# Kernel tuning notes

Hardware: AMD Instinct MI355X
Metric: run time of the kernel (lower is better)

## Reference

```python
import jax, jax.numpy as jnp
import numpy as np

R_CUT = 5.0
L_MAX = 3
N_MAX = (8, 7, 6, 5)  # n_max per angular order l (Laplacian-eigenstate-like, shrinking with l)
EPS = 1e-12


def _radial_basis(r):
    """r: [E] -> [E, N_MAX[0]] sine radial basis with smooth cosine cutoff.
    R_n(r) = f_cut(r) * sin((n+1) pi r / r_cut) / r, n = 0..n_max-1."""
    n = jnp.arange(1, N_MAX[0] + 1, dtype=r.dtype)  # (n+1)
    fcut = jnp.where(r < R_CUT, 0.5 * (jnp.cos(jnp.pi * r / R_CUT) + 1.0), 0.0)
    rb = jnp.sin(n[None, :] * (jnp.pi / R_CUT) * r[:, None]) / (r[:, None] + EPS)
    return rb * fcut[:, None]


def _spherical_harmonics(v, r):
    """v: [E,3], r: [E] -> tuple of real SH arrays ([E,1],[E,3],[E,5],[E,7]), m = -l..l."""
    ir = 1.0 / (r + EPS)
    x, y, z = v[:, 0] * ir, v[:, 1] * ir, v[:, 2] * ir
    pi = np.pi
    x2, y2, z2 = x * x, y * y, z * z
    # l = 0
    y0 = jnp.full_like(r, 0.5 * np.sqrt(1.0 / pi))[:, None]
    # l = 1
    c1 = np.sqrt(3.0 / (4.0 * pi))
    y1 = jnp.stack([c1 * y, c1 * z, c1 * x], axis=-1)
    # l = 2
    y2b = jnp.stack([
        0.5 * np.sqrt(15.0 / pi) * x * y,
        0.5 * np.sqrt(15.0 / pi) * y * z,
        0.25 * np.sqrt(5.0 / pi) * (2.0 * z2 - x2 - y2),
        0.5 * np.sqrt(15.0 / pi) * x * z,
        0.25 * np.sqrt(15.0 / pi) * (x2 - y2),
    ], axis=-1)
    # l = 3
    y3b = jnp.stack([
        0.25 * np.sqrt(35.0 / (2.0 * pi)) * y * (3.0 * x2 - y2),
        0.5 * np.sqrt(105.0 / pi) * x * y * z,
        0.25 * np.sqrt(21.0 / (2.0 * pi)) * y * (4.0 * z2 - x2 - y2),
        0.25 * np.sqrt(7.0 / pi) * z * (2.0 * z2 - 3.0 * x2 - 3.0 * y2),
        0.25 * np.sqrt(21.0 / (2.0 * pi)) * x * (4.0 * z2 - x2 - y2),
        0.25 * np.sqrt(105.0 / pi) * z * (x2 - y2),
        0.25 * np.sqrt(35.0 / (2.0 * pi)) * x * (x2 - 3.0 * y2),
    ], axis=-1)
    return (y0, y1, y2b, y3b)


def setup_inputs() -> dict:
    key = jax.random.key(0)
    E = 1_000_000
    vectors = 1.5 * jax.random.normal(key, (E, 3), dtype=jnp.float32)
    return {"vectors": vectors}


def reference(vectors):
    # vectors: [E, 3] bare cartesian edge vectors
    r = jnp.sqrt(jnp.sum(vectors * vectors, axis=-1))  # [E]
    rb = _radial_basis(r)                               # [E, N_MAX[0]]
    sh = _spherical_harmonics(vectors, r)               # per-l [E, 2l+1]
    # vector_expansion_l = radial_l[:, None, :] * sh_l[:, :, None] -> [E, 2l+1, n_max_l]
    blocks = tuple(sh[l][:, :, None] * rb[:, None, :N_MAX[l]] for l in range(L_MAX + 1))
    return blocks
```

## Files before the change

kernel.cpp:

```cpp
#include <hip/hip_runtime.h>
#include <math.h>


#define RCUT 5.0f
#define EPSF 1e-12f

typedef float fx4 __attribute__((ext_vector_type(4)));

template <int S>
__device__ __forceinline__ void stage_flush(float* __restrict__ lw,
                                            const float* __restrict__ vals,
                                            int lane,
                                            fx4* __restrict__ g4) {
#pragma unroll
  for (int i = 0; i < S; ++i) lw[lane * S + i] = vals[i];
  const fx4* l4 = reinterpret_cast<const fx4*>(lw);
  constexpr int NF4 = 16 * S;
  constexpr int NITER = (NF4 + 63) / 64;
#pragma unroll
  for (int it = 0; it < NITER; ++it) {
    int k = lane + it * 64;
    if ((NF4 % 64 == 0) || k < NF4) __builtin_nontemporal_store(l4[k], &g4[k]);
  }
}

__global__ __launch_bounds__(256) void vexp_kernel(const float* __restrict__ v,
                                                   float* __restrict__ out, int E) {
  __shared__ fx4 lbuf[4][560];
  const int lane = threadIdx.x & 63;
  const int wave = threadIdx.x >> 6;
  const long long e0 = ((long long)blockIdx.x * 4 + wave) * 64;
  if (e0 >= E) return;
  const bool fullwave = (e0 + 64 <= (long long)E);
  const int e = (int)e0 + lane;
  const bool valid = e < E;

  float x = 0.0f, y = 0.0f, z = 0.0f;
  if (valid) {
    x = v[3 * (size_t)e + 0];
    y = v[3 * (size_t)e + 1];
    z = v[3 * (size_t)e + 2];
  }

  float r2 = x * x + y * y + z * z;
  float r = sqrtf(r2);
  float ir = 1.0f / (r + EPSF);

  float theta = (3.14159265358979323846f / RCUT) * r;
  float s = __sinf(theta);
  float c = __cosf(theta);
  float fcut = (r < RCUT) ? 0.5f * (c + 1.0f) : 0.0f;
  float g = fcut * ir;

  float rb[8];
  {
    float twoc = 2.0f * c;
    float sp = 0.0f, sn = s;
    rb[0] = sn * g;
#pragma unroll
    for (int n = 1; n < 8; ++n) {
      float s2 = twoc * sn - sp;
      sp = sn;
      sn = s2;
      rb[n] = sn * g;
    }
  }

  float ux = x * ir, uy = y * ir, uz = z * ir;
  float xx = ux * ux, yy = uy * uy, zz = uz * uz;

  const float c1 = 0.48860251190291992f;
  float sh1[3] = {c1 * uy, c1 * uz, c1 * ux};

  const float c2a = 1.09254843059207907f;
  const float c2b = 0.31539156525252001f;
  const float c2c = 0.54627421529603953f;
  float sh2[5] = {c2a * ux * uy, c2a * uy * uz, c2b * (2.0f * zz - xx - yy),
                  c2a * ux * uz, c2c * (xx - yy)};

  const float c3a = 0.59004358992664352f;
  const float c3b = 2.89061144264055405f;
  const float c3c = 0.45704579946446574f;
  const float c3d = 0.37317633259011546f;
  const float c3e = 1.44530572132027702f;
  float sh3[7] = {c3a * uy * (3.0f * xx - yy),
                  c3b * ux * uy * uz,
                  c3c * uy * (4.0f * zz - xx - yy),
                  c3d * uz * (2.0f * zz - 3.0f * xx - 3.0f * yy),
                  c3c * ux * (4.0f * zz - xx - yy),
                  c3e * uz * (xx - yy),
                  c3a * ux * (xx - 3.0f * yy)};

  const size_t E_ = (size_t)E;
  float* lw = reinterpret_cast<float*>(lbuf[wave]);
  float vals[35];

  const float y0c = 0.28209479177387814f;
#pragma unroll
  for (int n = 0; n < 8; ++n) vals[n] = y0c * rb[n];
  if (fullwave) {
    stage_flush<8>(lw, vals, lane, reinterpret_cast<fx4*>(out + (size_t)e0 * 8));
  } else if (valid) {
    float* o = out + (size_t)e * 8;
#pragma unroll
    for (int i = 0; i < 8; ++i) o[i] = vals[i];
  }

#pragma unroll
  for (int m = 0; m < 3; ++m)
#pragma unroll
    for (int n = 0; n < 7; ++n) vals[m * 7 + n] = sh1[m] * rb[n];
  if (fullwave) {
    stage_flush<21>(lw, vals, lane,
                    reinterpret_cast<fx4*>(out + 8 * E_ + (size_t)e0 * 21));
  } else if (valid) {
    float* o = out + 8 * E_ + (size_t)e * 21;
#pragma unroll
    for (int i = 0; i < 21; ++i) o[i] = vals[i];
  }

#pragma unroll
  for (int m = 0; m < 5; ++m)
#pragma unroll
    for (int n = 0; n < 6; ++n) vals[m * 6 + n] = sh2[m] * rb[n];
  if (fullwave) {
    stage_flush<30>(lw, vals, lane,
                    reinterpret_cast<fx4*>(out + 29 * E_ + (size_t)e0 * 30));
  } else if (valid) {
    float* o = out + 29 * E_ + (size_t)e * 30;
#pragma unroll
    for (int i = 0; i < 30; ++i) o[i] = vals[i];
  }

#pragma unroll
  for (int m = 0; m < 7; ++m)
#pragma unroll
    for (int n = 0; n < 5; ++n) vals[m * 5 + n] = sh3[m] * rb[n];
  if (fullwave) {
    stage_flush<35>(lw, vals, lane,
                    reinterpret_cast<fx4*>(out + 59 * E_ + (size_t)e0 * 35));
  } else if (valid) {
    float* o = out + 59 * E_ + (size_t)e * 35;
#pragma unroll
    for (int i = 0; i < 35; ++i) o[i] = vals[i];
  }
}

extern "C" void kernel_launch(void* const* d_in, const int* in_sizes, int n_in,
                              void* d_out, int out_size, void* d_ws, size_t ws_size,
                              hipStream_t stream) {
  const float* v = (const float*)d_in[0];
  float* out = (float*)d_out;
  int E = in_sizes[0] / 3;
  int waves = (E + 63) / 64;
  int grid = (waves + 3) / 4;
  vexp_kernel<<<grid, 256, 0, stream>>>(v, out, E);
}
```

Measured before the change: 74.86 us.

## Remap workgroups to contiguous chunks per XCD and vectorize l=0 LDS staging

Block IDs are remapped so that each of the 8 XCDs (round-robin dispatch) handles a contiguous range of edges, which is meant to improve write locality per XCD and L2/memory channel behavior. The l=0 block now writes two fx4 values per lane into LDS with a permuted slot layout instead of eight scalar stores, cutting LDS store instructions. The rest is variable renaming. The remap assumes 8-way round-robin dispatch across XCDs.

```diff
diff --git a/kernel.cpp b/kernel.cpp
--- a/kernel.cpp
+++ b/kernel.cpp
@@ -25,31 +25,38 @@
 }
 
 __global__ __launch_bounds__(256) void vexp_kernel(const float* __restrict__ v,
-                                                   float* __restrict__ out, int E) {
+                                                   float* __restrict__ out, int E,
+                                                   int nwg) {
   __shared__ fx4 lbuf[4][560];
   const int lane = threadIdx.x & 63;
   const int wave = threadIdx.x >> 6;
-  const long long e0 = ((long long)blockIdx.x * 4 + wave) * 64;
+
+  int x = blockIdx.x & 7;
+  int i = blockIdx.x >> 3;
+  int q = nwg >> 3, r = nwg & 7;
+  int wg = (x < r) ? (x * (q + 1) + i) : (r * (q + 1) + (x - r) * q + i);
+
+  const long long e0 = ((long long)wg * 4 + wave) * 64;
   if (e0 >= E) return;
   const bool fullwave = (e0 + 64 <= (long long)E);
   const int e = (int)e0 + lane;
   const bool valid = e < E;
 
-  float x = 0.0f, y = 0.0f, z = 0.0f;
+  float xc = 0.0f, yc = 0.0f, zc = 0.0f;
   if (valid) {
-    x = v[3 * (size_t)e + 0];
-    y = v[3 * (size_t)e + 1];
-    z = v[3 * (size_t)e + 2];
+    xc = v[3 * (size_t)e + 0];
+    yc = v[3 * (size_t)e + 1];
+    zc = v[3 * (size_t)e + 2];
   }
 
-  float r2 = x * x + y * y + z * z;
-  float r = sqrtf(r2);
-  float ir = 1.0f / (r + EPSF);
+  float r2 = xc * xc + yc * yc + zc * zc;
+  float rr = sqrtf(r2);
+  float ir = 1.0f / (rr + EPSF);
 
-  float theta = (3.14159265358979323846f / RCUT) * r;
+  float theta = (3.14159265358979323846f / RCUT) * rr;
   float s = __sinf(theta);
   float c = __cosf(theta);
-  float fcut = (r < RCUT) ? 0.5f * (c + 1.0f) : 0.0f;
+  float fcut = (rr < RCUT) ? 0.5f * (c + 1.0f) : 0.0f;
   float g = fcut * ir;
 
   float rb[8];
@@ -66,7 +73,7 @@
     }
   }
 
-  float ux = x * ir, uy = y * ir, uz = z * ir;
+  float ux = xc * ir, uy = yc * ir, uz = zc * ir;
   float xx = ux * ux, yy = uy * uy, zz = uz * uz;
 
   const float c1 = 0.48860251190291992f;
@@ -93,17 +100,26 @@
 
   const size_t E_ = (size_t)E;
   float* lw = reinterpret_cast<float*>(lbuf[wave]);
+  fx4* l4 = lbuf[wave];
   float vals[35];
 
   const float y0c = 0.28209479177387814f;
+  if (fullwave) {
+    fx4 a0 = {y0c * rb[0], y0c * rb[1], y0c * rb[2], y0c * rb[3]};
+    fx4 b0 = {y0c * rb[4], y0c * rb[5], y0c * rb[6], y0c * rb[7]};
+    l4[lane] = a0;
+    l4[64 + lane] = b0;
+    fx4* g4 = reinterpret_cast<fx4*>(out + (size_t)e0 * 8);
 #pragma unroll
-  for (int n = 0; n < 8; ++n) vals[n] = y0c * rb[n];
-  if (fullwave) {
-    stage_flush<8>(lw, vals, lane, reinterpret_cast<fx4*>(out + (size_t)e0 * 8));
+    for (int it = 0; it < 2; ++it) {
+      int k = lane + it * 64;
+      int slot = ((k & 1) << 6) + (k >> 1);
+      __builtin_nontemporal_store(l4[slot], &g4[k]);
+    }
   } else if (valid) {
     float* o = out + (size_t)e * 8;
 #pragma unroll
-    for (int i = 0; i < 8; ++i) o[i] = vals[i];
+    for (int n = 0; n < 8; ++n) o[n] = y0c * rb[n];
   }
 
 #pragma unroll
@@ -116,7 +132,7 @@
   } else if (valid) {
     float* o = out + 8 * E_ + (size_t)e * 21;
 #pragma unroll
-    for (int i = 0; i < 21; ++i) o[i] = vals[i];
+    for (int i2 = 0; i2 < 21; ++i2) o[i2] = vals[i2];
   }
 
 #pragma unroll
@@ -129,7 +145,7 @@
   } else if (valid) {
     float* o = out + 29 * E_ + (size_t)e * 30;
 #pragma unroll
-    for (int i = 0; i < 30; ++i) o[i] = vals[i];
+    for (int i2 = 0; i2 < 30; ++i2) o[i2] = vals[i2];
   }
 
 #pragma unroll
@@ -142,7 +158,7 @@
   } else if (valid) {
     float* o = out + 59 * E_ + (size_t)e * 35;
 #pragma unroll
-    for (int i = 0; i < 35; ++i) o[i] = vals[i];
+    for (int i2 = 0; i2 < 35; ++i2) o[i2] = vals[i2];
   }
 }
 
@@ -154,5 +170,5 @@
   int E = in_sizes[0] / 3;
   int waves = (E + 63) / 64;
   int grid = (waves + 3) / 4;
-  vexp_kernel<<<grid, 256, 0, stream>>>(v, out, E);
+  vexp_kernel<<<grid, 256, 0, stream>>>(v, out, E, grid);
 }
```

Result: no change. 76.33 us (+2.0%).

## Split fused kernel into four per-angular-order kernels with smaller LDS staging

Applied to the files above, without the earlier changes.

Replaces the single kernel that computes and writes all four output blocks with four launches: a direct float4-store kernel for l=0 and a templated kernel per l=1..3 that stages only that section in LDS. Each kernel's LDS footprint and register count shrink, which is meant to raise occupancy and keep more stores in flight. The cost is reading the input vectors and recomputing r, the radial basis and the trig four times, plus three extra kernel launches.

```diff
diff --git a/kernel.cpp b/kernel.cpp
--- a/kernel.cpp
+++ b/kernel.cpp
@@ -7,26 +7,50 @@
 
 typedef float fx4 __attribute__((ext_vector_type(4)));
 
-template <int S>
-__device__ __forceinline__ void stage_flush(float* __restrict__ lw,
-                                            const float* __restrict__ vals,
-                                            int lane,
-                                            fx4* __restrict__ g4) {
+__device__ __forceinline__ void radial(float rr, float ir, float rb[8]) {
+  float theta = (3.14159265358979323846f / RCUT) * rr;
+  float s = __sinf(theta);
+  float c = __cosf(theta);
+  float fcut = (rr < RCUT) ? 0.5f * (c + 1.0f) : 0.0f;
+  float g = fcut * ir;
+  float twoc = 2.0f * c;
+  float sp = 0.0f, sn = s;
+  rb[0] = sn * g;
 #pragma unroll
-  for (int i = 0; i < S; ++i) lw[lane * S + i] = vals[i];
-  const fx4* l4 = reinterpret_cast<const fx4*>(lw);
-  constexpr int NF4 = 16 * S;
-  constexpr int NITER = (NF4 + 63) / 64;
-#pragma unroll
-  for (int it = 0; it < NITER; ++it) {
-    int k = lane + it * 64;
-    if ((NF4 % 64 == 0) || k < NF4) __builtin_nontemporal_store(l4[k], &g4[k]);
+  for (int n = 1; n < 8; ++n) {
+    float s2 = twoc * sn - sp;
+    sp = sn;
+    sn = s2;
+    rb[n] = sn * g;
   }
 }
 
-__global__ __launch_bounds__(256) void vexp_kernel(const float* __restrict__ v,
-                                                   float* __restrict__ out, int E) {
-  __shared__ fx4 lbuf[4][560];
+__global__ __launch_bounds__(256) void vexp_s0(const float* __restrict__ v,
+                                               float* __restrict__ out,
+                                               long long n4) {
+  long long tid = (long long)blockIdx.x * blockDim.x + threadIdx.x;
+  if (tid >= n4) return;
+  long long e = tid >> 1;
+  int half = (int)(tid & 1);
+  float x = v[3 * e + 0], y = v[3 * e + 1], z = v[3 * e + 2];
+  float rr = sqrtf(x * x + y * y + z * z);
+  float ir = 1.0f / (rr + EPSF);
+  float rb[8];
+  radial(rr, ir, rb);
+  const float y0c = 0.28209479177387814f;
+  int o = 4 * half;
+  fx4 val = {y0c * rb[o], y0c * rb[o + 1], y0c * rb[o + 2], y0c * rb[o + 3]};
+  __builtin_nontemporal_store(val, &reinterpret_cast<fx4*>(out)[tid]);
+}
+
+template <int L>
+__global__ __launch_bounds__(256) void vexp_sec(const float* __restrict__ v,
+                                                float* __restrict__ secbase,
+                                                int E) {
+  constexpr int M = 2 * L + 1;
+  constexpr int NM = 8 - L;
+  constexpr int S = M * NM;
+  __shared__ fx4 lbuf[4][16 * S];
   const int lane = threadIdx.x & 63;
   const int wave = threadIdx.x >> 6;
   const long long e0 = ((long long)blockIdx.x * 4 + wave) * 64;
@@ -41,108 +65,67 @@
     y = v[3 * (size_t)e + 1];
     z = v[3 * (size_t)e + 2];
   }
-
-  float r2 = x * x + y * y + z * z;
-  float r = sqrtf(r2);
-  float ir = 1.0f / (r + EPSF);
-
-  float theta = (3.14159265358979323846f / RCUT) * r;
-  float s = __sinf(theta);
-  float c = __cosf(theta);
-  float fcut = (r < RCUT) ? 0.5f * (c + 1.0f) : 0.0f;
-  float g = fcut * ir;
-
+  float rr = sqrtf(x * x + y * y + z * z);
+  float ir = 1.0f / (rr + EPSF);
   float rb[8];
-  {
-    float twoc = 2.0f * c;
-    float sp = 0.0f, sn = s;
-    rb[0] = sn * g;
-#pragma unroll
-    for (int n = 1; n < 8; ++n) {
-      float s2 = twoc * sn - sp;
-      sp = sn;
-      sn = s2;
-      rb[n] = sn * g;
-    }
-  }
+  radial(rr, ir, rb);
 
   float ux = x * ir, uy = y * ir, uz = z * ir;
   float xx = ux * ux, yy = uy * uy, zz = uz * uz;
 
-  const float c1 = 0.48860251190291992f;
-  float sh1[3] = {c1 * uy, c1 * uz, c1 * ux};
-
-  const float c2a = 1.09254843059207907f;
-  const float c2b = 0.31539156525252001f;
-  const float c2c = 0.54627421529603953f;
-  float sh2[5] = {c2a * ux * uy, c2a * uy * uz, c2b * (2.0f * zz - xx - yy),
-                  c2a * ux * uz, c2c * (xx - yy)};
-
-  const float c3a = 0.59004358992664352f;
-  const float c3b = 2.89061144264055405f;
-  const float c3c = 0.45704579946446574f;
-  const float c3d = 0.37317633259011546f;
-  const float c3e = 1.44530572132027702f;
-  float sh3[7] = {c3a * uy * (3.0f * xx - yy),
-                  c3b * ux * uy * uz,
-                  c3c * uy * (4.0f * zz - xx - yy),
-                  c3d * uz * (2.0f * zz - 3.0f * xx - 3.0f * yy),
-                  c3c * ux * (4.0f * zz - xx - yy),
-                  c3e * uz * (xx - yy),
-                  c3a * ux * (xx - 3.0f * yy)};
-
-  const size_t E_ = (size_t)E;
-  float* lw = reinterpret_cast<float*>(lbuf[wave]);
-  float vals[35];
-
-  const float y0c = 0.28209479177387814f;
-#pragma unroll
-  for (int n = 0; n < 8; ++n) vals[n] = y0c * rb[n];
-  if (fullwave) {
-    stage_flush<8>(lw, vals, lane, reinterpret_cast<fx4*>(out + (size_t)e0 * 8));
-  } else if (valid) {
-    float* o = out + (size_t)e * 8;
-#pragma unroll
-    for (int i = 0; i < 8; ++i) o[i] = vals[i];
+  float sh[M];
+  if constexpr (L == 1) {
+    const float c1 = 0.48860251190291992f;
+    sh[0] = c1 * uy;
+    sh[1] = c1 * uz;
+    sh[2] = c1 * ux;
+  } else if constexpr (L == 2) {
+    const float c2a = 1.09254843059207907f;
+    const float c2b = 0.31539156525252001f;
+    const float c2c = 0.54627421529603953f;
+    sh[0] = c2a * ux * uy;
+    sh[1] = c2a * uy * uz;
+    sh[2] = c2b * (2.0f * zz - xx - yy);
+    sh[3] = c2a * ux * uz;
+    sh[4] = c2c * (xx - yy);
+  } else {
+    const float c3a = 0.59004358992664352f;
+    const float c3b = 2.89061144264055405f;
+    const float c3c = 0.45704579946446574f;
+    const float c3d = 0.37317633259011546f;
+    const float c3e = 1.44530572132027702f;
+    sh[0] = c3a * uy * (3.0f * xx - yy);
+    sh[1] = c3b * ux * uy * uz;
+    sh[2] = c3c * uy * (4.0f * zz - xx - yy);
+    sh[3] = c3d * uz * (2.0f * zz - 3.0f * xx - 3.0f * yy);
+    sh[4] = c3c * ux * (4.0f * zz - xx - yy);
+    sh[5] = c3e * uz * (xx - yy);
+    sh[6] = c3a * ux * (xx - 3.0f * yy);
   }
 
+  float vals[S];
 #pragma unroll
-  for (int m = 0; m < 3; ++m)
+  for (int m = 0; m < M; ++m)
 #pragma unroll
-    for (int n = 0; n < 7; ++n) vals[m * 7 + n] = sh1[m] * rb[n];
+    for (int n = 0; n < NM; ++n) vals[m * NM + n] = sh[m] * rb[n];
+
   if (fullwave) {
-    stage_flush<21>(lw, vals, lane,
-                    reinterpret_cast<fx4*>(out + 8 * E_ + (size_t)e0 * 21));
+    float* lw = reinterpret_cast<float*>(lbuf[wave]);
+#pragma unroll
+    for (int i = 0; i < S; ++i) lw[lane * S + i] = vals[i];
+    const fx4* l4 = lbuf[wave];
+    fx4* g4 = reinterpret_cast<fx4*>(secbase + (size_t)e0 * S);
+    constexpr int NF4 = 16 * S;
+    constexpr int NITER = (NF4 + 63) / 64;
+#pragma unroll
+    for (int it = 0; it < NITER; ++it) {
+      int k = lane + it * 64;
+      if ((NF4 % 64 == 0) || k < NF4) __builtin_nontemporal_store(l4[k], &g4[k]);
+    }
   } else if (valid) {
-    float* o = out + 8 * E_ + (size_t)e * 21;
+    float* o = secbase + (size_t)e * S;
 #pragma unroll
-    for (int i = 0; i < 21; ++i) o[i] = vals[i];
-  }
-
-#pragma unroll
-  for (int m = 0; m < 5; ++m)
-#pragma unroll
-    for (int n = 0; n < 6; ++n) vals[m * 6 + n] = sh2[m] * rb[n];
-  if (fullwave) {
-    stage_flush<30>(lw, vals, lane,
-                    reinterpret_cast<fx4*>(out + 29 * E_ + (size_t)e0 * 30));
-  } else if (valid) {
-    float* o = out + 29 * E_ + (size_t)e * 30;
-#pragma unroll
-    for (int i = 0; i < 30; ++i) o[i] = vals[i];
-  }
-
-#pragma unroll
-  for (int m = 0; m < 7; ++m)
-#pragma unroll
-    for (int n = 0; n < 5; ++n) vals[m * 5 + n] = sh3[m] * rb[n];
-  if (fullwave) {
-    stage_flush<35>(lw, vals, lane,
-                    reinterpret_cast<fx4*>(out + 59 * E_ + (size_t)e0 * 35));
-  } else if (valid) {
-    float* o = out + 59 * E_ + (size_t)e * 35;
-#pragma unroll
-    for (int i = 0; i < 35; ++i) o[i] = vals[i];
+    for (int i = 0; i < S; ++i) o[i] = vals[i];
   }
 }
 
@@ -152,7 +135,15 @@
   const float* v = (const float*)d_in[0];
   float* out = (float*)d_out;
   int E = in_sizes[0] / 3;
+  size_t E_ = (size_t)E;
+
+  long long n4 = 2LL * E;
+  int grid0 = (int)((n4 + 255) / 256);
+  vexp_s0<<<grid0, 256, 0, stream>>>(v, out, n4);
+
   int waves = (E + 63) / 64;
   int grid = (waves + 3) / 4;
-  vexp_kernel<<<grid, 256, 0, stream>>>(v, out, E);
+  vexp_sec<1><<<grid, 256, 0, stream>>>(v, out + 8 * E_, E);
+  vexp_sec<2><<<grid, 256, 0, stream>>>(v, out + 29 * E_, E);
+  vexp_sec<3><<<grid, 256, 0, stream>>>(v, out + 59 * E_, E);
 }
```

New measurement: 74.67 us. Within noise of the previous version (-0.3%).
